# Kernel tuning notes

Hardware: AMD Instinct MI355X
Metric: run time of the kernel (lower is better)

Reference implementation:

```python
import jax, jax.numpy as jnp
import numpy as np

SDF_THRESHOLD = 5e-05
N_ITERATIONS = 6
N_FIX_ITERATIONS = 3
N_RAYS = 32768
HIDDEN = 128


def setup_inputs() -> dict:
    key = jax.random.key(0)
    ks = jax.random.split(key, 5)
    rays_d = jax.random.normal(ks[0], (N_RAYS, 3), jnp.float32)
    rays_d = rays_d / jnp.linalg.norm(rays_d, axis=-1, keepdims=True)
    rays_o = jax.random.normal(ks[1], (N_RAYS, 3), jnp.float32)
    W1 = jax.random.normal(ks[2], (3, HIDDEN), jnp.float32) * (1.0 / np.sqrt(3.0))
    b1 = jnp.zeros((HIDDEN,), jnp.float32)
    W2 = jax.random.normal(ks[3], (HIDDEN, HIDDEN), jnp.float32) * (1.0 / np.sqrt(HIDDEN))
    b2 = jnp.zeros((HIDDEN,), jnp.float32)
    W3 = jax.random.normal(ks[4], (HIDDEN, 1), jnp.float32) * (1.0 / np.sqrt(HIDDEN))
    b3 = jnp.zeros((1,), jnp.float32)
    return {"rays_d": rays_d, "rays_o": rays_o, "W1": W1, "b1": b1,
            "W2": W2, "b2": b2, "W3": W3, "b3": b3}


def _sdf(pts, W1, b1, W2, b2, W3, b3):
    # pts: (..., 3) -> sdf values (...)
    h = jax.nn.softplus(pts @ W1 + b1)
    h = jax.nn.softplus(h @ W2 + b2)
    return (h @ W3 + b3)[..., 0]


def _trace(rays_d, rays_o, W1, b1, W2, b2, W3, b3):
    sdf = lambda p: _sdf(p, W1, b1, W2, b2, W3, b3)
    n = rays_d.reshape(-1, 3).shape[0]
    directions = jnp.broadcast_to(rays_d.reshape(-1, 3)[None], (2, n, 3))
    origins = jnp.broadcast_to(rays_o.reshape(-1, 3)[None], (2, n, 3))
    z_vals = jnp.zeros((2, n), rays_d.dtype)
    points = z_vals[..., None] * directions + origins
    next_sdf = sdf(points)                     # (2, n)
    mask_unfinished = jnp.ones((2, n), bool)
    # sign: +1 for channel 0, -1 for channel 1
    sign = jnp.concatenate([jnp.ones((1, n), rays_d.dtype),
                            -jnp.ones((1, n), rays_d.dtype)], axis=0)

    for _ in range(N_ITERATIONS):
        sdf_vals = jnp.where(mask_unfinished, next_sdf, 0.0)
        sdf_vals = jnp.where(sdf_vals <= SDF_THRESHOLD, 0.0, sdf_vals)
        mask_unfinished = jnp.logical_and(mask_unfinished, sdf_vals > SDF_THRESHOLD)
        z_vals = z_vals + sign * sdf_vals
        points = z_vals[..., None] * directions + origins
        next_sdf = jnp.where(mask_unfinished, sdf(points), 0.0)
        # fix_overshoot: bisection-style correction where sdf went negative
        fmask = next_sdf < 0
        for i in range(N_FIX_ITERATIONS):
            step = 0.5 / (2.0 ** i)
            z_vals = jnp.where(fmask, z_vals - step * sign * sdf_vals, z_vals)
            points = jnp.where(fmask[..., None],
                               z_vals[..., None] * directions + origins, points)
            next_sdf = jnp.where(fmask, sdf(points), next_sdf)
            fmask = next_sdf < 0
        mask_unfinished = jnp.logical_and(mask_unfinished,
                                          (z_vals[0] < z_vals[1])[None, :])

    # final top-of-loop mask update before break (iteration == n_iterations)
    sdf_vals = jnp.where(mask_unfinished, next_sdf, 0.0)
    sdf_vals = jnp.where(sdf_vals <= SDF_THRESHOLD, 0.0, sdf_vals)
    mask_unfinished = jnp.logical_and(mask_unfinished, sdf_vals > SDF_THRESHOLD)
    return points, z_vals, mask_unfinished


def reference(rays_d, rays_o, W1, b1, W2, b2, W3, b3):
    return _trace(rays_d, rays_o, W1, b1, W2, b2, W3, b3)
```

## Files before the change

kernel.cpp:

```cpp
#include <hip/hip_runtime.h>

#define NRAYS 32768
#define THRS  5e-5f

typedef float f32x4 __attribute__((ext_vector_type(4)));
typedef short s16x8 __attribute__((ext_vector_type(8)));

#define WB(s,ct,kb) ((((s)*8+(ct))*4+(kb))*1024)
#define T1B  98304
#define B2B  100352
#define W3B  100864
#define B3B  101376
#define PXB  101392
#define PYB  102416
#define PZB  103440
#define SDFB 104464
#define CNTB 105488
#define LDSZ 105616

__device__ __forceinline__ float softplus_f(float x){
  const float L2E = 1.44269504088896340f;
  const float LN2 = 0.69314718055994531f;
  float y = __builtin_amdgcn_exp2f(-fabsf(x) * L2E);
  float l = __builtin_amdgcn_logf(1.0f + y);
  return fmaf(LN2, l, fmaxf(x, 0.0f));
}

__device__ __forceinline__ float bf16tof(unsigned short h){
  return __uint_as_float(((unsigned int)h) << 16);
}
__device__ __forceinline__ void split3(float h, unsigned short& a0,
                                       unsigned short& a1, unsigned short& a2){
  a0 = (unsigned short)(__float_as_uint(h) >> 16);
  const float r1 = h - bf16tof(a0);
  a1 = (unsigned short)(__float_as_uint(r1) >> 16);
  const float r2 = r1 - bf16tof(a1);
  a2 = (unsigned short)(__float_as_uint(r2) >> 16);
}

__device__ __forceinline__ void eval_blockN(unsigned char* sm, int t, int nw){
  const int lane = t & 63;
  const int wave = t >> 6;
  const int l15  = lane & 15;
  const int lhi  = lane >> 4;

  if (wave < nw){
    float prx[2], pry[2], prz[2];
#pragma unroll
    for (int mt = 0; mt < 2; ++mt){
      const int row = wave*32 + mt*16 + l15;
      prx[mt] = ((const float*)(sm+PXB))[row];
      pry[mt] = ((const float*)(sm+PYB))[row];
      prz[mt] = ((const float*)(sm+PZB))[row];
    }

    f32x4 acc[2][8];
#pragma unroll
    for (int mt = 0; mt < 2; ++mt)
#pragma unroll
      for (int ct = 0; ct < 8; ++ct){
        f32x4 zv = {0.f,0.f,0.f,0.f};
        acc[mt][ct] = zv;
      }

#pragma unroll
    for (int kb = 0; kb < 4; ++kb){
      s16x8 A0[2], A1[2], A2[2];
#pragma unroll
      for (int u = 0; u < 8; ++u){
        const int k = kb*32 + lhi*8 + u;
        const float4 t1 = ((const float4*)(sm+T1B))[k];
#pragma unroll
        for (int mt = 0; mt < 2; ++mt){
          const float pre = fmaf(prx[mt], t1.x,
                            fmaf(pry[mt], t1.y,
                            fmaf(prz[mt], t1.z, t1.w)));
          const float h = softplus_f(pre);
          unsigned short uh, um, ul;
          split3(h, uh, um, ul);
          A0[mt][u] = (short)uh; A1[mt][u] = (short)um; A2[mt][u] = (short)ul;
        }
      }
#pragma unroll
      for (int ct = 0; ct < 8; ++ct){
        const s16x8 B0  = *(const s16x8*)(sm + WB(0,ct,kb) + lane*16);
        const s16x8 B1  = *(const s16x8*)(sm + WB(1,ct,kb) + lane*16);
        const s16x8 B2w = *(const s16x8*)(sm + WB(2,ct,kb) + lane*16);
#pragma unroll
        for (int mt = 0; mt < 2; ++mt){
          f32x4 a = acc[mt][ct];
          a = __builtin_amdgcn_mfma_f32_16x16x32_bf16(A0[mt], B0,  a, 0,0,0);
          a = __builtin_amdgcn_mfma_f32_16x16x32_bf16(A0[mt], B1,  a, 0,0,0);
          a = __builtin_amdgcn_mfma_f32_16x16x32_bf16(A1[mt], B0,  a, 0,0,0);
          a = __builtin_amdgcn_mfma_f32_16x16x32_bf16(A0[mt], B2w, a, 0,0,0);
          a = __builtin_amdgcn_mfma_f32_16x16x32_bf16(A1[mt], B1,  a, 0,0,0);
          a = __builtin_amdgcn_mfma_f32_16x16x32_bf16(A2[mt], B0,  a, 0,0,0);
          acc[mt][ct] = a;
        }
      }
    }

    float b2v[8], w3v[8];
#pragma unroll
    for (int ct = 0; ct < 8; ++ct){
      const int col = ct*16 + l15;
      b2v[ct] = ((const float*)(sm+B2B))[col];
      w3v[ct] = ((const float*)(sm+W3B))[col];
    }
#pragma unroll
    for (int mt = 0; mt < 2; ++mt){
#pragma unroll
      for (int i = 0; i < 4; ++i){
        float v = 0.f;
#pragma unroll
        for (int ct = 0; ct < 8; ++ct)
          v = fmaf(softplus_f(acc[mt][ct][i] + b2v[ct]), w3v[ct], v);
        v += __shfl_xor(v, 1);
        v += __shfl_xor(v, 2);
        v += __shfl_xor(v, 4);
        v += __shfl_xor(v, 8);
        if (l15 == 0)
          ((float*)(sm+SDFB))[wave*32 + mt*16 + lhi*4 + i] = v;
      }
    }
  }
  __syncthreads();
}

__device__ __forceinline__ float do_eval(unsigned char* sm, int t, bool flag,
                                         float px, float py, float pz,
                                         float prev, int evalIdx){
  const int lane = t & 63;
  int* cnt = (int*)(sm + CNTB);
  const unsigned long long bal = __ballot(flag);
  const int pc = __popcll(bal);
  int base = 0;
  if (pc){
    int old = 0;
    if (lane == 0) old = atomicAdd(&cnt[evalIdx], pc);
    base = __shfl(old, 0);
  }
  const int slot = base + __popcll(bal & ((1ULL << lane) - 1ULL));
  if (flag){
    ((float*)(sm+PXB))[slot] = px;
    ((float*)(sm+PYB))[slot] = py;
    ((float*)(sm+PZB))[slot] = pz;
  }
  __syncthreads();
  const int total = cnt[evalIdx];
  if (total == 0) return prev;
  eval_blockN(sm, t, (total + 31) >> 5);
  float r = prev;
  if (flag)
    r = ((const float*)(sm+SDFB))[slot] + *((const float*)(sm+B3B));
  return r;
}

__global__ __launch_bounds__(512, 2)
void trace_kernel(const float* __restrict__ rays_d, const float* __restrict__ rays_o,
                  const float* __restrict__ W1, const float* __restrict__ b1,
                  const float* __restrict__ W2, const float* __restrict__ b2,
                  const float* __restrict__ W3, const float* __restrict__ b3,
                  float* __restrict__ out)
{
  __shared__ __align__(16) unsigned char sm[LDSZ];
  const int t = threadIdx.x;

  const bool own = (t < 256);
  const int chan = blockIdx.x * 256 + (t & 255);
  const int ray  = chan >> 1;
  const int c01  = chan & 1;
  const float sgn = c01 ? -1.0f : 1.0f;

  float dx=0, dy=0, dz=0, ox=0, oy=0, oz=0;
  if (own){
    dx = rays_d[ray*3+0]; dy = rays_d[ray*3+1]; dz = rays_d[ray*3+2];
    ox = rays_o[ray*3+0]; oy = rays_o[ray*3+1]; oz = rays_o[ray*3+2];
  }

  for (int si = t; si < 2048; si += 512){
    const int k    = si & 127;
    const int joct = si >> 7;
    s16x8 vh, vm, vl;
#pragma unroll
    for (int jj = 0; jj < 8; ++jj){
      const float w = W2[(joct*8 + jj)*128 + k];
      unsigned short uh, um, ul;
      split3(w, uh, um, ul);
      vh[jj] = (short)uh; vm[jj] = (short)um; vl[jj] = (short)ul;
    }
    const int ct = k >> 4, kb = joct >> 2;
    const int slot = ((joct & 3)*16 + (k & 15))*16;
    *(s16x8*)(sm + WB(0,ct,kb) + slot) = vh;
    *(s16x8*)(sm + WB(1,ct,kb) + slot) = vm;
    *(s16x8*)(sm + WB(2,ct,kb) + slot) = vl;
  }
  if (t < 128){
    ((float4*)(sm+T1B))[t] = make_float4(W1[t], W1[128+t], W1[256+t], b1[t]);
    ((float*)(sm+B2B))[t] = b2[t];
    ((float*)(sm+W3B))[t] = W3[t];
  }
  if (t == 0) *((float*)(sm+B3B)) = b3[0];
  if (t < 32) ((int*)(sm+CNTB))[t] = 0;

  if (own && (c01 == 0)){
    const int slot = t >> 1;
    ((float*)(sm+PXB))[slot] = ox;
    ((float*)(sm+PYB))[slot] = oy;
    ((float*)(sm+PZB))[slot] = oz;
  }
  __syncthreads();
  eval_blockN(sm, t, 4);
  float next_sdf = own
      ? ((const float*)(sm+SDFB))[(t & 255) >> 1] + *((const float*)(sm+B3B))
      : 0.f;

  float z = 0.f, sv = 0.f;
  float px = ox, py = oy, pz = oz;
  bool m = own;
  int evalIdx = 0;

  for (int it = 0; it < 6; ++it){
    sv = m ? next_sdf : 0.f;
    sv = (sv <= THRS) ? 0.f : sv;
    m = m && (sv > THRS);
    z = fmaf(sgn, sv, z);
    px = fmaf(z, dx, ox); py = fmaf(z, dy, oy); pz = fmaf(z, dz, oz);

    next_sdf = do_eval(sm, t, m, px, py, pz, 0.f, evalIdx++);

    bool fm = own && (next_sdf < 0.f);
    float step = 0.5f;
    for (int fi = 0; fi < 3; ++fi){
      if (fm){
        z = fmaf(-step*sgn, sv, z);
        px = fmaf(z, dx, ox); py = fmaf(z, dy, oy); pz = fmaf(z, dz, oz);
      }
      next_sdf = do_eval(sm, t, fm, px, py, pz, next_sdf, evalIdx++);
      fm = own && (next_sdf < 0.f);
      step *= 0.5f;
    }

    const float zo = __shfl_xor(z, 1);
    const bool pair = c01 ? (zo < z) : (z < zo);
    m = m && pair;

    if (!__syncthreads_or((int)m)) break;
  }

  if (own){
    sv = m ? next_sdf : 0.f;
    sv = (sv <= THRS) ? 0.f : sv;
    m = m && (sv > THRS);

    const size_t pb = (size_t)c01 * NRAYS * 3 + (size_t)ray * 3;
    out[pb+0] = px; out[pb+1] = py; out[pb+2] = pz;
    out[2*NRAYS*3 + (size_t)c01*NRAYS + ray] = z;
    out[2*NRAYS*3 + 2*NRAYS + (size_t)c01*NRAYS + ray] = m ? 1.f : 0.f;
  }
}

extern "C" void kernel_launch(void* const* d_in, const int* in_sizes, int n_in,
                              void* d_out, int out_size, void* d_ws, size_t ws_size,
                              hipStream_t stream) {
  const float* rays_d = (const float*)d_in[0];
  const float* rays_o = (const float*)d_in[1];
  const float* W1 = (const float*)d_in[2];
  const float* b1 = (const float*)d_in[3];
  const float* W2 = (const float*)d_in[4];
  const float* b2 = (const float*)d_in[5];
  const float* W3 = (const float*)d_in[6];
  const float* b3 = (const float*)d_in[7];
  float* out = (float*)d_out;
  (void)d_ws; (void)ws_size;

  trace_kernel<<<256, 512, 0, stream>>>(
      rays_d, rays_o, W1, b1, W2, b2, W3, b3, out);
}
```

Baseline: 25.26 us.

## Speculatively evaluate all three overshoot-fix points in one batched SDF pass

New measurement: 24.94 us. Within noise of the previous version (-1.3%).

```diff
diff --git a/kernel.cpp b/kernel.cpp
--- a/kernel.cpp
+++ b/kernel.cpp
@@ -156,6 +156,46 @@
   return r;
 }
 
+__device__ __forceinline__ void do_eval3(unsigned char* sm, int t, bool flag,
+    float p1x, float p1y, float p1z,
+    float p2x, float p2y, float p2z,
+    float p3x, float p3y, float p3z,
+    int evalIdx, float& e1, float& e2, float& e3, bool& usedSpec){
+  const int lane = t & 63;
+  int* cnt = (int*)(sm + CNTB);
+  const unsigned long long bal = __ballot(flag);
+  const int pc = __popcll(bal);
+  int base = 0;
+  if (pc){
+    int old = 0;
+    if (lane == 0) old = atomicAdd(&cnt[evalIdx], pc);
+    base = __shfl(old, 0);
+  }
+  const int r = base + __popcll(bal & ((1ULL << lane) - 1ULL));
+  if (flag && 3*r + 2 < 256){
+    float* PX = (float*)(sm+PXB);
+    float* PY = (float*)(sm+PYB);
+    float* PZ = (float*)(sm+PZB);
+    PX[3*r+0] = p1x; PY[3*r+0] = p1y; PZ[3*r+0] = p1z;
+    PX[3*r+1] = p2x; PY[3*r+1] = p2y; PZ[3*r+1] = p2z;
+    PX[3*r+2] = p3x; PY[3*r+2] = p3y; PZ[3*r+2] = p3z;
+  }
+  __syncthreads();
+  const int total = cnt[evalIdx] * 3;
+  e1 = 0.f; e2 = 0.f; e3 = 0.f;
+  if (total == 0){ usedSpec = true; return; }
+  if (total > 256){ usedSpec = false; return; }
+  eval_blockN(sm, t, (total + 31) >> 5);
+  usedSpec = true;
+  if (flag){
+    const float b3v = *((const float*)(sm+B3B));
+    const float* S = (const float*)(sm+SDFB);
+    e1 = S[3*r+0] + b3v;
+    e2 = S[3*r+1] + b3v;
+    e3 = S[3*r+2] + b3v;
+  }
+}
+
 __global__ __launch_bounds__(512, 2)
 void trace_kernel(const float* __restrict__ rays_d, const float* __restrict__ rays_o,
                   const float* __restrict__ W1, const float* __restrict__ b1,
@@ -227,19 +267,39 @@
     z = fmaf(sgn, sv, z);
     px = fmaf(z, dx, ox); py = fmaf(z, dy, oy); pz = fmaf(z, dz, oz);
 
-    next_sdf = do_eval(sm, t, m, px, py, pz, 0.f, evalIdx++);
+    next_sdf = do_eval(sm, t, m, px, py, pz, 0.f, evalIdx);
 
     bool fm = own && (next_sdf < 0.f);
-    float step = 0.5f;
-    for (int fi = 0; fi < 3; ++fi){
+
+    const float z1p = fmaf(-0.5f  * sgn, sv, z);
+    const float z2p = fmaf(-0.25f * sgn, sv, z1p);
+    const float z3p = fmaf(-0.125f* sgn, sv, z2p);
+    float e1, e2, e3; bool usedSpec;
+    do_eval3(sm, t, fm,
+             fmaf(z1p,dx,ox), fmaf(z1p,dy,oy), fmaf(z1p,dz,oz),
+             fmaf(z2p,dx,ox), fmaf(z2p,dy,oy), fmaf(z2p,dz,oz),
+             fmaf(z3p,dx,ox), fmaf(z3p,dy,oy), fmaf(z3p,dz,oz),
+             evalIdx + 1, e1, e2, e3, usedSpec);
+    if (usedSpec){
       if (fm){
-        z = fmaf(-step*sgn, sv, z);
+        if (e1 >= 0.f)      { z = z1p; next_sdf = e1; }
+        else if (e2 >= 0.f) { z = z2p; next_sdf = e2; }
+        else                { z = z3p; next_sdf = e3; }
         px = fmaf(z, dx, ox); py = fmaf(z, dy, oy); pz = fmaf(z, dz, oz);
       }
-      next_sdf = do_eval(sm, t, fm, px, py, pz, next_sdf, evalIdx++);
-      fm = own && (next_sdf < 0.f);
-      step *= 0.5f;
-    }
+    } else {
+      float step = 0.5f;
+      for (int fi = 0; fi < 3; ++fi){
+        if (fm){
+          z = fmaf(-step*sgn, sv, z);
+          px = fmaf(z, dx, ox); py = fmaf(z, dy, oy); pz = fmaf(z, dz, oz);
+        }
+        next_sdf = do_eval(sm, t, fm, px, py, pz, next_sdf, evalIdx + 2 + fi);
+        fm = own && (next_sdf < 0.f);
+        step *= 0.5f;
+      }
+    }
+    evalIdx += 5;
 
     const float zo = __shfl_xor(z, 1);
     const bool pair = c01 ? (zo < z) : (z < zo);
```
